# Kernel optimization log

Hardware: AMD Instinct MI355X
Metric: run time of the kernel (lower is better)

Reference implementation:

```python
import jax, jax.numpy as jnp
import numpy as np

TOP_K = 2
EPS = 1e-10


def setup_inputs() -> dict:
    key = jax.random.key(0)
    k1, k2 = jax.random.split(key)
    B, S, D, E = 4, 4096, 4096, 64
    hidden_states = jax.random.normal(k1, (B, S, D), dtype=jnp.float32)
    # router weight, scaled like a standard linear init
    w_router = jax.random.normal(k2, (D, E), dtype=jnp.float32) / np.sqrt(D)
    return {"hidden_states": hidden_states, "w_router": w_router}


def reference(hidden_states, w_router):
    # router: [B,S,D] x [D,E] -> [B,S,E]
    router_logits = jnp.einsum("bsd,de->bse", hidden_states, w_router)
    # balanced_assignment: softmax, global load, penalty, adjusted top-k
    routing_probs = jax.nn.softmax(router_logits, axis=-1)
    current_load = routing_probs.sum(axis=(0, 1))            # [E]
    load_penalty = current_load / (current_load.mean() + EPS)  # [E]
    adjusted_logits = router_logits - jnp.log(load_penalty + EPS)
    _, expert_indices = jax.lax.top_k(adjusted_logits, TOP_K)  # [B,S,top_k]
    return adjusted_logits, expert_indices
```

## Files before the change

kernel.cpp:

```cpp
#include <hip/hip_runtime.h>
#include <math.h>

#define ROWS 16384
#define DD   4096
#define EE   64
#define EPSF 1e-10f

#define BM    64
#define KT    32
#define NKT   (DD / KT)
#define WTILE 12288

typedef __attribute__((ext_vector_type(8))) short short8;
typedef __attribute__((ext_vector_type(4))) float f32x4;
typedef __attribute__((ext_vector_type(4))) unsigned u32x4;

__device__ __forceinline__ void split3x8(const float f[8], u32x4& w0,
                                         u32x4& w1, u32x4& w2) {
#pragma unroll
  for (int i = 0; i < 4; ++i) {
    float fa = f[2 * i], fb = f[2 * i + 1];
    unsigned ua = __float_as_uint(fa), ub = __float_as_uint(fb);
    unsigned ra = ua + 0x7fffu + ((ua >> 16) & 1u);
    unsigned rb = ub + 0x7fffu + ((ub >> 16) & 1u);
    w0[i] = (rb & 0xffff0000u) | (ra >> 16);
    fa -= __uint_as_float(ra & 0xffff0000u);
    fb -= __uint_as_float(rb & 0xffff0000u);
    ua = __float_as_uint(fa); ub = __float_as_uint(fb);
    ra = ua + 0x7fffu + ((ua >> 16) & 1u);
    rb = ub + 0x7fffu + ((ub >> 16) & 1u);
    w1[i] = (rb & 0xffff0000u) | (ra >> 16);
    fa -= __uint_as_float(ra & 0xffff0000u);
    fb -= __uint_as_float(rb & 0xffff0000u);
    ua = __float_as_uint(fa); ub = __float_as_uint(fb);
    ra = ua + 0x7fffu + ((ua >> 16) & 1u);
    rb = ub + 0x7fffu + ((ub >> 16) & 1u);
    w2[i] = (rb & 0xffff0000u) | (ra >> 16);
  }
}

__device__ __forceinline__ void dma16(const void* g, void* l) {
  __builtin_amdgcn_global_load_lds(
      (const __attribute__((address_space(1))) unsigned int*)g,
      (__attribute__((address_space(3))) unsigned int*)l, 16, 0, 0);
}

__global__ __launch_bounds__(256) void k_wsplit(const float* __restrict__ wr,
                                                unsigned char* __restrict__ out,
                                                float* __restrict__ g_load) {
  const int kt = blockIdx.x;
  const int t = threadIdx.x;
  const int lane = t & 63, wv = t >> 6;
  if (blockIdx.x == 0 && t < 64) g_load[t] = 0.f;
  float f[8];
  const float* wp = wr + (size_t)(kt * 32 + wv * 8) * EE + lane;
#pragma unroll
  for (int j = 0; j < 8; ++j) f[j] = wp[(size_t)j * EE];
  u32x4 w0, w1, w2;
  split3x8(f, w0, w1, w2);
  const int et = lane >> 4;
  const int lp = wv * 16 + (lane & 15);
  unsigned char* base = out + (size_t)kt * WTILE + et * 1024 + lp * 16;
  *(u32x4*)(base + 0 * 4096) = w0;
  *(u32x4*)(base + 1 * 4096) = w1;
  *(u32x4*)(base + 2 * 4096) = w2;
}

__global__ __launch_bounds__(512) void k_gemm(
    const float* __restrict__ h, const unsigned char* __restrict__ wsp,
    float* __restrict__ logits, float* __restrict__ g_load) {
  __shared__ alignas(16) unsigned char smem[2 * WTILE];

  const int t = threadIdx.x;
  const int lane = t & 63;
  const int wv = t >> 6;
  const int mt = wv >> 1;
  const int eh = wv & 1;
  const int row0 = blockIdx.x * BM;

  f32x4 acc[2] = {};

  const float* ap =
      h + (size_t)(row0 + mt * 16 + (lane & 15)) * DD + (lane >> 4) * 8;

  const int slot0 = wv * 1024 + lane * 16;

  float4 cur0, cur1, nxt0, nxt1;
  cur0 = *(const float4*)(ap);
  cur1 = *(const float4*)(ap + 4);
  dma16(wsp + slot0, smem + slot0);
  if (wv < 4) dma16(wsp + 8192 + slot0, smem + 8192 + slot0);

  for (int kt = 0; kt < NKT; ++kt) {
    const int buf = kt & 1;
    const unsigned char* lb = smem + buf * WTILE;
    asm volatile("s_waitcnt vmcnt(0)" ::: "memory");
    __syncthreads();

    if (kt + 1 < NKT) {
      const float* p = ap + (size_t)(kt + 1) * KT;
      nxt0 = *(const float4*)(p);
      nxt1 = *(const float4*)(p + 4);
      const unsigned char* ws = wsp + (size_t)(kt + 1) * WTILE;
      unsigned char* nb = smem + (buf ^ 1) * WTILE;
      dma16(ws + slot0, nb + slot0);
      if (wv < 4) dma16(ws + 8192 + slot0, nb + 8192 + slot0);
    }

    short8 bf[3][2];
#pragma unroll
    for (int p = 0; p < 3; ++p)
#pragma unroll
      for (int e = 0; e < 2; ++e)
        bf[p][e] = *(const short8*)&lb[p * 4096 + (eh * 2 + e) * 1024 +
                                       lane * 16];

    const float af[8] = {cur0.x, cur0.y, cur0.z, cur0.w,
                         cur1.x, cur1.y, cur1.z, cur1.w};
    u32x4 q0, q1, q2;
    split3x8(af, q0, q1, q2);
    const short8 ah0 = __builtin_bit_cast(short8, q0);
    const short8 ah1 = __builtin_bit_cast(short8, q1);
    const short8 ah2 = __builtin_bit_cast(short8, q2);
#pragma unroll
    for (int e = 0; e < 2; ++e) {
      f32x4 c = acc[e];
      c = __builtin_amdgcn_mfma_f32_16x16x32_bf16(ah0, bf[0][e], c, 0, 0, 0);
      c = __builtin_amdgcn_mfma_f32_16x16x32_bf16(ah0, bf[1][e], c, 0, 0, 0);
      c = __builtin_amdgcn_mfma_f32_16x16x32_bf16(ah1, bf[0][e], c, 0, 0, 0);
      c = __builtin_amdgcn_mfma_f32_16x16x32_bf16(ah0, bf[2][e], c, 0, 0, 0);
      c = __builtin_amdgcn_mfma_f32_16x16x32_bf16(ah1, bf[1][e], c, 0, 0, 0);
      c = __builtin_amdgcn_mfma_f32_16x16x32_bf16(ah2, bf[0][e], c, 0, 0, 0);
      acc[e] = c;
    }

    if (kt + 1 < NKT) { cur0 = nxt0; cur1 = nxt1; }
  }

  __syncthreads();
  float* sl = (float*)smem;
  {
    const int rb = mt * 16 + (lane >> 4) * 4;
    const int cb = eh * 32 + (lane & 15);
#pragma unroll
    for (int e = 0; e < 2; ++e)
#pragma unroll
      for (int r = 0; r < 4; ++r)
        sl[(rb + r) * 68 + cb + e * 16] = acc[e][r];
  }
  __syncthreads();

  float accp = 0.f;
#pragma unroll
  for (int i = 0; i < 8; ++i) {
    const int row = wv * 8 + i;
    const float x = sl[row * 68 + lane];
    float m = x;
#pragma unroll
    for (int off = 32; off > 0; off >>= 1) m = fmaxf(m, __shfl_xor(m, off, 64));
    const float p = __expf(x - m);
    float s = p;
#pragma unroll
    for (int off = 32; off > 0; off >>= 1) s += __shfl_xor(s, off, 64);
    accp += p / s;
    logits[(size_t)(row0 + row) * EE + lane] = x;
  }
  float* red = sl + 64 * 68;
  red[wv * 64 + lane] = accp;
  __syncthreads();
  if (wv == 0) {
    float s = 0.f;
#pragma unroll
    for (int j = 0; j < 8; ++j) s += red[j * 64 + lane];
    atomicAdd(&g_load[lane], s);
  }
}

__global__ __launch_bounds__(256) void k_top2(float* __restrict__ logits,
                                              const float* __restrict__ g_load,
                                              float* __restrict__ idx_out) {
  int t = threadIdx.x;
  int lane = t & 63;
  int wv = t >> 6;
  int row = blockIdx.x * 4 + wv;

  float v0 = g_load[lane];
  float s0 = v0;
#pragma unroll
  for (int off = 32; off > 0; off >>= 1) s0 += __shfl_xor(s0, off, 64);
  float lp = logf(v0 / (s0 * (1.f / 64.f) + EPSF) + EPSF);

  size_t base = (size_t)row * EE;
  float a = logits[base + lane] - lp;
  logits[base + lane] = a;

  float v = a;
  int idx = lane;
#pragma unroll
  for (int off = 32; off > 0; off >>= 1) {
    float ov = __shfl_xor(v, off, 64);
    int oi = __shfl_xor(idx, off, 64);
    if (ov > v || (ov == v && oi < idx)) { v = ov; idx = oi; }
  }
  int i1 = idx;

  float a2 = (lane == i1) ? -INFINITY : a;
  v = a2;
  idx = lane;
#pragma unroll
  for (int off = 32; off > 0; off >>= 1) {
    float ov = __shfl_xor(v, off, 64);
    int oi = __shfl_xor(idx, off, 64);
    if (ov > v || (ov == v && oi < idx)) { v = ov; idx = oi; }
  }
  int i2 = idx;

  if (lane == 0) {
    idx_out[(size_t)row * 2 + 0] = (float)i1;
    idx_out[(size_t)row * 2 + 1] = (float)i2;
  }
}

extern "C" void kernel_launch(void* const* d_in, const int* in_sizes, int n_in,
                              void* d_out, int out_size, void* d_ws,
                              size_t ws_size, hipStream_t stream) {
  const float* h = (const float*)d_in[0];
  const float* wr = (const float*)d_in[1];
  float* out = (float*)d_out;
  float* logits = out;
  float* idx_out = out + (size_t)ROWS * EE;
  float* g_load = (float*)d_ws;
  unsigned char* wsp = (unsigned char*)d_ws + 512;

  k_wsplit<<<DD / KT, 256, 0, stream>>>(wr, wsp, g_load);
  k_gemm<<<ROWS / BM, 512, 0, stream>>>(h, wsp, logits, g_load);
  k_top2<<<ROWS / 4, 256, 0, stream>>>(logits, g_load, idx_out);
}
```

Baseline: 449.6 us.

## Halve GEMM row tile, double K step, and use 256-thread blocks

The router GEMM block now covers 32 rows with 4 waves instead of 64 rows with 8 waves. Each iteration processes a 64-wide K slice as two sub-steps, loading two pre-split weight tiles per stage through global-to-LDS DMA. This doubles the grid, so more blocks can be resident per CU, and halves the number of barriers per K sweep while keeping more A loads in flight per thread. The cost is that each weight tile is reused across fewer rows, so weight traffic from L2 doubles. It also adds register pressure from the extra prefetched A vectors.

After: 426.4 us. -5.1%, faster.

```diff
diff --git a/kernel.cpp b/kernel.cpp
--- a/kernel.cpp
+++ b/kernel.cpp
@@ -6,10 +6,11 @@
 #define EE   64
 #define EPSF 1e-10f
 
-#define BM    64
-#define KT    32
+#define BM    32
+#define KT    64
 #define NKT   (DD / KT)
 #define WTILE 12288
+#define BTILE (2 * WTILE)
 
 typedef __attribute__((ext_vector_type(8))) short short8;
 typedef __attribute__((ext_vector_type(4))) float f32x4;
@@ -66,10 +67,10 @@
   *(u32x4*)(base + 2 * 4096) = w2;
 }
 
-__global__ __launch_bounds__(512) void k_gemm(
+__global__ __launch_bounds__(256) void k_gemm(
     const float* __restrict__ h, const unsigned char* __restrict__ wsp,
     float* __restrict__ logits, float* __restrict__ g_load) {
-  __shared__ alignas(16) unsigned char smem[2 * WTILE];
+  __shared__ alignas(16) unsigned char smem[2 * BTILE];
 
   const int t = threadIdx.x;
   const int lane = t & 63;
@@ -82,61 +83,73 @@
 
   const float* ap =
       h + (size_t)(row0 + mt * 16 + (lane & 15)) * DD + (lane >> 4) * 8;
-
-  const int slot0 = wv * 1024 + lane * 16;
-
-  float4 cur0, cur1, nxt0, nxt1;
-  cur0 = *(const float4*)(ap);
-  cur1 = *(const float4*)(ap + 4);
-  dma16(wsp + slot0, smem + slot0);
-  if (wv < 4) dma16(wsp + 8192 + slot0, smem + 8192 + slot0);
+  const int dmaoff = t * 16;
+
+  float4 c0, c1, c2, c3, n0, n1, n2, n3;
+
+#pragma unroll
+  for (int i = 0; i < 6; ++i)
+    dma16(wsp + i * 4096 + dmaoff, smem + i * 4096 + dmaoff);
+  c0 = *(const float4*)(ap);
+  c1 = *(const float4*)(ap + 4);
+  c2 = *(const float4*)(ap + 32);
+  c3 = *(const float4*)(ap + 36);
 
   for (int kt = 0; kt < NKT; ++kt) {
     const int buf = kt & 1;
-    const unsigned char* lb = smem + buf * WTILE;
     asm volatile("s_waitcnt vmcnt(0)" ::: "memory");
     __syncthreads();
 
     if (kt + 1 < NKT) {
+      const unsigned char* ws = wsp + (size_t)(kt + 1) * BTILE;
+      unsigned char* nb = smem + (buf ^ 1) * BTILE;
+#pragma unroll
+      for (int i = 0; i < 6; ++i)
+        dma16(ws + i * 4096 + dmaoff, nb + i * 4096 + dmaoff);
       const float* p = ap + (size_t)(kt + 1) * KT;
-      nxt0 = *(const float4*)(p);
-      nxt1 = *(const float4*)(p + 4);
-      const unsigned char* ws = wsp + (size_t)(kt + 1) * WTILE;
-      unsigned char* nb = smem + (buf ^ 1) * WTILE;
-      dma16(ws + slot0, nb + slot0);
-      if (wv < 4) dma16(ws + 8192 + slot0, nb + 8192 + slot0);
+      n0 = *(const float4*)(p);
+      n1 = *(const float4*)(p + 4);
+      n2 = *(const float4*)(p + 32);
+      n3 = *(const float4*)(p + 36);
     }
 
-    short8 bf[3][2];
-#pragma unroll
-    for (int p = 0; p < 3; ++p)
-#pragma unroll
-      for (int e = 0; e < 2; ++e)
-        bf[p][e] = *(const short8*)&lb[p * 4096 + (eh * 2 + e) * 1024 +
-                                       lane * 16];
-
-    const float af[8] = {cur0.x, cur0.y, cur0.z, cur0.w,
-                         cur1.x, cur1.y, cur1.z, cur1.w};
-    u32x4 q0, q1, q2;
-    split3x8(af, q0, q1, q2);
-    const short8 ah0 = __builtin_bit_cast(short8, q0);
-    const short8 ah1 = __builtin_bit_cast(short8, q1);
-    const short8 ah2 = __builtin_bit_cast(short8, q2);
-#pragma unroll
-    for (int e = 0; e < 2; ++e) {
-      f32x4 c = acc[e];
-      c = __builtin_amdgcn_mfma_f32_16x16x32_bf16(ah0, bf[0][e], c, 0, 0, 0);
-      c = __builtin_amdgcn_mfma_f32_16x16x32_bf16(ah0, bf[1][e], c, 0, 0, 0);
-      c = __builtin_amdgcn_mfma_f32_16x16x32_bf16(ah1, bf[0][e], c, 0, 0, 0);
-      c = __builtin_amdgcn_mfma_f32_16x16x32_bf16(ah0, bf[2][e], c, 0, 0, 0);
-      c = __builtin_amdgcn_mfma_f32_16x16x32_bf16(ah1, bf[1][e], c, 0, 0, 0);
-      c = __builtin_amdgcn_mfma_f32_16x16x32_bf16(ah2, bf[0][e], c, 0, 0, 0);
-      acc[e] = c;
+    const unsigned char* lb = smem + buf * BTILE;
+#pragma unroll
+    for (int sub = 0; sub < 2; ++sub) {
+      const unsigned char* sb = lb + sub * WTILE;
+      short8 bf[3][2];
+#pragma unroll
+      for (int p = 0; p < 3; ++p)
+#pragma unroll
+        for (int e = 0; e < 2; ++e)
+          bf[p][e] =
+              *(const short8*)&sb[p * 4096 + (eh * 2 + e) * 1024 + lane * 16];
+
+      const float4 a0 = sub ? c2 : c0;
+      const float4 a1 = sub ? c3 : c1;
+      const float af[8] = {a0.x, a0.y, a0.z, a0.w, a1.x, a1.y, a1.z, a1.w};
+      u32x4 q0, q1, q2;
+      split3x8(af, q0, q1, q2);
+      const short8 ah0 = __builtin_bit_cast(short8, q0);
+      const short8 ah1 = __builtin_bit_cast(short8, q1);
+      const short8 ah2 = __builtin_bit_cast(short8, q2);
+#pragma unroll
+      for (int e = 0; e < 2; ++e) {
+        f32x4 c = acc[e];
+        c = __builtin_amdgcn_mfma_f32_16x16x32_bf16(ah0, bf[0][e], c, 0, 0, 0);
+        c = __builtin_amdgcn_mfma_f32_16x16x32_bf16(ah0, bf[1][e], c, 0, 0, 0);
+        c = __builtin_amdgcn_mfma_f32_16x16x32_bf16(ah1, bf[0][e], c, 0, 0, 0);
+        c = __builtin_amdgcn_mfma_f32_16x16x32_bf16(ah0, bf[2][e], c, 0, 0, 0);
+        c = __builtin_amdgcn_mfma_f32_16x16x32_bf16(ah1, bf[1][e], c, 0, 0, 0);
+        c = __builtin_amdgcn_mfma_f32_16x16x32_bf16(ah2, bf[0][e], c, 0, 0, 0);
+        acc[e] = c;
+      }
     }
 
-    if (kt + 1 < NKT) { cur0 = nxt0; cur1 = nxt1; }
-  }
-
+    if (kt + 1 < NKT) { c0 = n0; c1 = n1; c2 = n2; c3 = n3; }
+  }
+
+  asm volatile("s_waitcnt vmcnt(0)" ::: "memory");
   __syncthreads();
   float* sl = (float*)smem;
   {
@@ -165,13 +178,12 @@
     accp += p / s;
     logits[(size_t)(row0 + row) * EE + lane] = x;
   }
-  float* red = sl + 64 * 68;
+  float* red = sl + 32 * 68;
   red[wv * 64 + lane] = accp;
   __syncthreads();
   if (wv == 0) {
-    float s = 0.f;
-#pragma unroll
-    for (int j = 0; j < 8; ++j) s += red[j * 64 + lane];
+    float s = red[0 * 64 + lane] + red[1 * 64 + lane] + red[2 * 64 + lane] +
+              red[3 * 64 + lane];
     atomicAdd(&g_load[lane], s);
   }
 }
@@ -232,7 +244,7 @@
   float* g_load = (float*)d_ws;
   unsigned char* wsp = (unsigned char*)d_ws + 512;
 
-  k_wsplit<<<DD / KT, 256, 0, stream>>>(wr, wsp, g_load);
-  k_gemm<<<ROWS / BM, 512, 0, stream>>>(h, wsp, logits, g_load);
+  k_wsplit<<<DD / 32, 256, 0, stream>>>(wr, wsp, g_load);
+  k_gemm<<<ROWS / BM, 256, 0, stream>>>(h, wsp, logits, g_load);
   k_top2<<<ROWS / 4, 256, 0, stream>>>(logits, g_load, idx_out);
 }
```
